# Optimization experiments

Measured on AMD Instinct MI355X. Metric: run time of the kernel, lower is better.

The kernel has to match this reference:

```python
import jax, jax.numpy as jnp
import numpy as np


def setup_inputs() -> dict:
    key = jax.random.key(0)
    k1, k2 = jax.random.split(key)
    B, D = 8192, 256
    pred = jax.random.normal(k1, (B, D), dtype=jnp.float32)
    gt = jax.random.normal(k2, (B, D), dtype=jnp.float32)
    sigma = jnp.ones((), dtype=jnp.float32)  # learned scalar param (dim=1, mode='auto')
    return {"pred": pred, "gt": gt, "sigma": sigma}


def reference(pred, gt, sigma):
    # p, g: [B, D] (flatten from start_dim=1 is identity for 2D inputs)
    p = pred.reshape(pred.shape[0], -1)
    g = gt.reshape(gt.shape[0], -1)
    B, D = p.shape
    noise_var = sigma ** 2
    # MVN(mean=p_i, cov=noise_var*I).log_prob(g_j) in closed form:
    # -0.5 * ||g_j - p_i||^2 / noise_var - 0.5 * D * log(2*pi*noise_var)
    sq_dist = (
        jnp.sum(p * p, axis=-1)[:, None]
        + jnp.sum(g * g, axis=-1)[None, :]
        - 2.0 * (p @ g.T)
    )  # [B, B]
    log_norm = 0.5 * D * jnp.log(2.0 * jnp.pi * noise_var)
    logits = -0.5 * sq_dist / noise_var - log_norm  # [B, B], class dim = 1
    # cross_entropy(logits, arange(B)) = mean_i(-log_softmax(logits)[i, i])
    logp = jax.nn.log_softmax(logits, axis=1)
    loss = -jnp.mean(jnp.diagonal(logp))
    loss = loss * jax.lax.stop_gradient(2.0 * noise_var)
    return loss
```

## Files before the change

### kernel.cpp

```cpp
#include <hip/hip_runtime.h>
#include <hip/hip_fp8.h>


typedef float f32x4 __attribute__((ext_vector_type(4)));
typedef long llong2 __attribute__((ext_vector_type(2)));

#define LN2F 0.6931471805599453f
#define LOG2EF 1.4426950408889634f
#define NB 8192
#define ND 256
#define NCHUNK 32

#define AS1 __attribute__((address_space(1)))
#define AS3 __attribute__((address_space(3)))

__device__ __forceinline__ float fexp2(float x) {
#if __has_builtin(__builtin_amdgcn_exp2f)
  return __builtin_amdgcn_exp2f(x);
#else
  float r;
  asm("v_exp_f32 %0, %1\n\ts_nop 1" : "=v"(r) : "v"(x));
  return r;
#endif
}

__device__ __forceinline__ int pack4_fp8(float a, float b, float c, float d) {
#if __has_builtin(__builtin_amdgcn_cvt_pk_fp8_f32)
  int w = __builtin_amdgcn_cvt_pk_fp8_f32(a, b, 0, false);
  w = __builtin_amdgcn_cvt_pk_fp8_f32(c, d, w, true);
  return w;
#else
  unsigned b0 = __hip_fp8_e4m3(a).__x, b1 = __hip_fp8_e4m3(b).__x;
  unsigned b2 = __hip_fp8_e4m3(c).__x, b3 = __hip_fp8_e4m3(d).__x;
  return (int)(b0 | (b1 << 8) | (b2 << 16) | (b3 << 24));
#endif
}

__global__ __launch_bounds__(256) void vmse_prep(
    const float* __restrict__ pred, const float* __restrict__ gt,
    const float* __restrict__ sigma,
    unsigned char* __restrict__ Ah, unsigned char* __restrict__ Bh,
    float* __restrict__ diag, float* __restrict__ gnorm,
    float* __restrict__ ghs)
{
  const float nv = sigma[0] * sigma[0];
  const float s = LOG2EF / nv;
  const int row = blockIdx.x * 4 + (threadIdx.x >> 6);
  const int l = threadIdx.x & 63;
  const float4 p = *(const float4*)(pred + row * ND + l * 4);
  const float4 g = *(const float4*)(gt   + row * ND + l * 4);
  const int pw = pack4_fp8(p.x * s, p.y * s, p.z * s, p.w * s);
  const int gw = pack4_fp8(g.x, g.y, g.z, g.w);
  const int pos = (l >> 4) * 64 + ((l & 7) >> 1) * 16 + ((l >> 3) & 1) * 8 + (l & 1) * 4;
  *(int*)(Ah + row * ND + pos) = pw;
  *(int*)(Bh + row * ND + pos) = gw;
  float dd = p.x * g.x + p.y * g.y + p.z * g.z + p.w * g.w;
  float gg = g.x * g.x + g.y * g.y + g.z * g.z + g.w * g.w;
  #pragma unroll
  for (int off = 1; off < 64; off <<= 1) {
    dd += __shfl_xor(dd, off);
    gg += __shfl_xor(gg, off);
  }
  if (l == 0) {
    diag[row] = dd;
    gnorm[row] = gg;
    ghs[row] = -0.5f * s * gg;
  }
}

__device__ __forceinline__ void epi(const f32x4 z, float& m, float& l) {
  const float tmax = fmaxf(fmaxf(z[0], z[1]), fmaxf(z[2], z[3]));
  if (__any(tmax > m + 8.0f)) {
    const float nm = fmaxf(m, tmax);
    l *= fexp2(m - nm);
    m = nm;
  }
  l += (fexp2(z[0] - m) + fexp2(z[1] - m)) + (fexp2(z[2] - m) + fexp2(z[3] - m));
}

__global__ __launch_bounds__(512, 4) void vmse_main(
    const unsigned char* __restrict__ Ah, const unsigned char* __restrict__ Bh,
    const float* __restrict__ ghs, float* __restrict__ partial)
{
  __shared__ unsigned char lds[8][32 * 256];
  __shared__ float lds_ghs[256];
  const int tid = threadIdx.x;
  const int lane = tid & 63;
  const int wid = tid >> 6;
  const int rb = blockIdx.x & 31;
  const int ch = blockIdx.x >> 5;
  const int r15 = lane & 15;
  const int hi = lane >> 4;
  const int j0 = ch * 256;

  {
    const int r = wid * 4 + (lane >> 4);
    const int cg = (lane & 15) ^ (r & 7);
    const unsigned char* src = Bh + (size_t)(j0 + r) * ND + cg * 16;
    #pragma unroll
    for (int t = 0; t < 8; ++t)
      __builtin_amdgcn_global_load_lds(
          (const AS1 unsigned int*)(src + t * 8192),
          (AS3 unsigned int*)&lds[t][wid * 1024], 16, 0, 0);
  }
  if (tid < 256) lds_ghs[tid] = ghs[j0 + tid];

  long pf[2][8];
  #pragma unroll
  for (int ns = 0; ns < 2; ++ns) {
    const unsigned char* prow =
        Ah + (size_t)((rb * 256) + (wid * 32) + (ns * 16) + r15) * ND;
    #pragma unroll
    for (int kk2 = 0; kk2 < 4; ++kk2) {
      const llong2 v = *(const llong2*)(prow + kk2 * 64 + hi * 16);
      pf[ns][2 * kk2] = v[0];
      pf[ns][2 * kk2 + 1] = v[1];
    }
  }

  const int r7 = r15 & 7;
  const int r7lo = r7 & 3, r7hi = r7 >> 2;
  const int h2 = hi ^ r7lo;
  const char* base = (const char*)&lds[0][0] + r15 * 256 + h2 * 16;
  const char* pE = base + r7hi * 64;
  const char* pO = base + 64 - r7hi * 64;

  float m2[2], l2[2];
  #pragma unroll
  for (int ns = 0; ns < 2; ++ns) { m2[ns] = -3.0e38f; l2[ns] = 0.0f; }

  #define COMPUTE(PE, PO, gp)                                                \
    {                                                                        \
      _Pragma("unroll")                                                      \
      for (int ms = 0; ms < 2; ++ms) {                                       \
        const f32x4 gv = *(const f32x4*)((gp) + ms * 64 + hi * 16);          \
        f32x4 a0 = gv;                                                       \
        f32x4 a1 = gv;                                                       \
        const llong2 gA = *(const llong2*)((PE) + ms * 4096);                \
        const llong2 gB = *(const llong2*)((PO) + ms * 4096);                \
        const llong2 gC = *(const llong2*)((PE) + ms * 4096 + 128);          \
        const llong2 gD = *(const llong2*)((PO) + ms * 4096 + 128);          \
        const long gf[8] = {gA[0], gA[1], gB[0], gB[1],                      \
                            gC[0], gC[1], gD[0], gD[1]};                     \
        __builtin_amdgcn_s_setprio(1);                                       \
        _Pragma("unroll")                                                    \
        for (int kk = 0; kk < 8; ++kk) {                                     \
          a0 = __builtin_amdgcn_mfma_f32_16x16x32_fp8_fp8(gf[kk], pf[0][kk], a0, 0, 0, 0); \
          a1 = __builtin_amdgcn_mfma_f32_16x16x32_fp8_fp8(gf[kk], pf[1][kk], a1, 0, 0, 0); \
        }                                                                    \
        __builtin_amdgcn_s_setprio(0);                                       \
        epi(a0, m2[0], l2[0]);                                               \
        epi(a1, m2[1], l2[1]);                                               \
      }                                                                      \
    }

  __syncthreads();

  const char* pEc = pE;
  const char* pOc = pO;
  const char* gp = (const char*)lds_ghs;
  for (int tt = 0; tt < 4; ++tt) {
    COMPUTE(pEc, pOc, gp);
    COMPUTE(pEc + 8192, pOc + 8192, gp + 128);
    pEc += 16384; pOc += 16384; gp += 256;
  }

  #pragma unroll
  for (int ns = 0; ns < 2; ++ns) {
    float m = m2[ns], l = l2[ns];
    #pragma unroll
    for (int off = 16; off <= 32; off <<= 1) {
      const float om = __shfl_xor(m, off);
      const float ol = __shfl_xor(l, off);
      const float nm = fmaxf(m, om);
      l = l * fexp2(m - nm) + ol * fexp2(om - nm);
      m = nm;
    }
    if (hi == 0) {
      const int row = rb * 256 + wid * 32 + ns * 16 + r15;
      partial[row * NCHUNK + ch] = m + log2f(l);
    }
  }
}

__global__ __launch_bounds__(256) void vmse_combine(
    const float* __restrict__ partial, const float* __restrict__ diag,
    const float* __restrict__ gnorm, const float* __restrict__ sigma,
    float* __restrict__ bsum)
{
  const int r = blockIdx.x * 256 + threadIdx.x;
  const float nv = sigma[0] * sigma[0];
  float p[NCHUNK];
  float M = -3.0e38f;
  #pragma unroll
  for (int c = 0; c < NCHUNK; ++c) { p[c] = partial[r * NCHUNK + c]; M = fmaxf(M, p[c]); }
  float ssum = 0.f;
  #pragma unroll
  for (int c = 0; c < NCHUNK; ++c) ssum += exp2f(p[c] - M);
  const float lse2 = M + log2f(ssum);
  const float zii = (diag[r] - 0.5f * gnorm[r]) / nv;
  float contrib = LN2F * lse2 - zii;
  #pragma unroll
  for (int off = 1; off < 64; off <<= 1) contrib += __shfl_xor(contrib, off);
  __shared__ float wsum[4];
  if ((threadIdx.x & 63) == 0) wsum[threadIdx.x >> 6] = contrib;
  __syncthreads();
  if (threadIdx.x == 0)
    bsum[blockIdx.x] = (wsum[0] + wsum[1]) + (wsum[2] + wsum[3]);
}

__global__ __launch_bounds__(64) void vmse_final(
    const float* __restrict__ bsum, const float* __restrict__ sigma,
    float* __restrict__ out)
{
  const int lane = threadIdx.x;
  float v = (lane < 32) ? bsum[lane] : 0.f;
  #pragma unroll
  for (int off = 1; off < 64; off <<= 1) v += __shfl_xor(v, off);
  if (lane == 0) {
    const float nv = sigma[0] * sigma[0];
    out[0] = v * (2.0f * nv / (float)NB);
  }
}

extern "C" void kernel_launch(void* const* d_in, const int* in_sizes, int n_in,
                              void* d_out, int out_size, void* d_ws, size_t ws_size,
                              hipStream_t stream)
{
  const float* pred  = (const float*)d_in[0];
  const float* gt    = (const float*)d_in[1];
  const float* sigma = (const float*)d_in[2];
  char* ws = (char*)d_ws;
  unsigned char* Ah = (unsigned char*)(ws);
  unsigned char* Bh = (unsigned char*)(ws + (2u << 20));
  float* gnorm   = (float*)(ws + (4u << 20));
  float* diag    = (float*)(ws + (4u << 20) + (32u << 10));
  float* ghs     = (float*)(ws + (4u << 20) + (64u << 10));
  float* partial = (float*)(ws + (4u << 20) + (96u << 10));
  float* bsum    = (float*)(ws + (4u << 20) + (96u << 10) + (1u << 20));

  vmse_prep<<<NB / 4, 256, 0, stream>>>(pred, gt, sigma, Ah, Bh, diag, gnorm, ghs);
  vmse_main<<<32 * NCHUNK, 512, 0, stream>>>(Ah, Bh, ghs, partial);
  vmse_combine<<<NB / 256, 256, 0, stream>>>(partial, diag, gnorm, sigma, bsum);
  vmse_final<<<1, 64, 0, stream>>>(bsum, sigma, (float*)d_out);
}
```

Before: 45.26 us.

## Switch main GEMM from 16x16x32 to 32x32x16 FP8 MFMA tiles

Replaces the pair of 16x16x32 FP8 MFMA accumulators per wave with a single 32x32x16 MFMA accumulator covering 32 rows by 32 columns. To match the new fragment shape it changes the FP8 packing layout in the prep kernel, the LDS swizzle, and the per-lane A-fragment loads. The online log-sum-exp epilogue now works on 16-element accumulators with one cross-half shuffle merge. This should cut LDS fragment loads per MFMA and give higher MFMA throughput per instruction, at the cost of a larger accumulator and more exp work per epilogue step.

```diff
diff --git a/kernel.cpp b/kernel.cpp
--- a/kernel.cpp
+++ b/kernel.cpp
@@ -3,6 +3,7 @@
 
 
 typedef float f32x4 __attribute__((ext_vector_type(4)));
+typedef float f32x16 __attribute__((ext_vector_type(16)));
 typedef long llong2 __attribute__((ext_vector_type(2)));
 
 #define LN2F 0.6931471805599453f
@@ -51,7 +52,7 @@
   const float4 g = *(const float4*)(gt   + row * ND + l * 4);
   const int pw = pack4_fp8(p.x * s, p.y * s, p.z * s, p.w * s);
   const int gw = pack4_fp8(g.x, g.y, g.z, g.w);
-  const int pos = (l >> 4) * 64 + ((l & 7) >> 1) * 16 + ((l >> 3) & 1) * 8 + (l & 1) * 4;
+  const int pos = (l >> 3) * 32 + ((l >> 1) & 1) * 16 + ((l >> 2) & 1) * 8 + (l & 1) * 4;
   *(int*)(Ah + row * ND + pos) = pw;
   *(int*)(Bh + row * ND + pos) = gw;
   float dd = p.x * g.x + p.y * g.y + p.z * g.z + p.w * g.w;
@@ -66,16 +67,6 @@
     gnorm[row] = gg;
     ghs[row] = -0.5f * s * gg;
   }
-}
-
-__device__ __forceinline__ void epi(const f32x4 z, float& m, float& l) {
-  const float tmax = fmaxf(fmaxf(z[0], z[1]), fmaxf(z[2], z[3]));
-  if (__any(tmax > m + 8.0f)) {
-    const float nm = fmaxf(m, tmax);
-    l *= fexp2(m - nm);
-    m = nm;
-  }
-  l += (fexp2(z[0] - m) + fexp2(z[1] - m)) + (fexp2(z[2] - m) + fexp2(z[3] - m));
 }
 
 __global__ __launch_bounds__(512, 4) void vmse_main(
@@ -89,8 +80,8 @@
   const int wid = tid >> 6;
   const int rb = blockIdx.x & 31;
   const int ch = blockIdx.x >> 5;
-  const int r15 = lane & 15;
-  const int hi = lane >> 4;
+  const int r31 = lane & 31;
+  const int hi = lane >> 5;
   const int j0 = ch * 256;
 
   {
@@ -105,80 +96,82 @@
   }
   if (tid < 256) lds_ghs[tid] = ghs[j0 + tid];
 
-  long pf[2][8];
-  #pragma unroll
-  for (int ns = 0; ns < 2; ++ns) {
-    const unsigned char* prow =
-        Ah + (size_t)((rb * 256) + (wid * 32) + (ns * 16) + r15) * ND;
-    #pragma unroll
-    for (int kk2 = 0; kk2 < 4; ++kk2) {
-      const llong2 v = *(const llong2*)(prow + kk2 * 64 + hi * 16);
-      pf[ns][2 * kk2] = v[0];
-      pf[ns][2 * kk2 + 1] = v[1];
-    }
-  }
-
-  const int r7 = r15 & 7;
-  const int r7lo = r7 & 3, r7hi = r7 >> 2;
-  const int h2 = hi ^ r7lo;
-  const char* base = (const char*)&lds[0][0] + r15 * 256 + h2 * 16;
-  const char* pE = base + r7hi * 64;
-  const char* pO = base + 64 - r7hi * 64;
-
-  float m2[2], l2[2];
-  #pragma unroll
-  for (int ns = 0; ns < 2; ++ns) { m2[ns] = -3.0e38f; l2[ns] = 0.0f; }
-
-  #define COMPUTE(PE, PO, gp)                                                \
-    {                                                                        \
-      _Pragma("unroll")                                                      \
-      for (int ms = 0; ms < 2; ++ms) {                                       \
-        const f32x4 gv = *(const f32x4*)((gp) + ms * 64 + hi * 16);          \
-        f32x4 a0 = gv;                                                       \
-        f32x4 a1 = gv;                                                       \
-        const llong2 gA = *(const llong2*)((PE) + ms * 4096);                \
-        const llong2 gB = *(const llong2*)((PO) + ms * 4096);                \
-        const llong2 gC = *(const llong2*)((PE) + ms * 4096 + 128);          \
-        const llong2 gD = *(const llong2*)((PO) + ms * 4096 + 128);          \
-        const long gf[8] = {gA[0], gA[1], gB[0], gB[1],                      \
-                            gC[0], gC[1], gD[0], gD[1]};                     \
-        __builtin_amdgcn_s_setprio(1);                                       \
-        _Pragma("unroll")                                                    \
-        for (int kk = 0; kk < 8; ++kk) {                                     \
-          a0 = __builtin_amdgcn_mfma_f32_16x16x32_fp8_fp8(gf[kk], pf[0][kk], a0, 0, 0, 0); \
-          a1 = __builtin_amdgcn_mfma_f32_16x16x32_fp8_fp8(gf[kk], pf[1][kk], a1, 0, 0, 0); \
-        }                                                                    \
-        __builtin_amdgcn_s_setprio(0);                                       \
-        epi(a0, m2[0], l2[0]);                                               \
-        epi(a1, m2[1], l2[1]);                                               \
-      }                                                                      \
-    }
+  long pf[16];
+  {
+    const unsigned char* prow = Ah + (size_t)((rb * 256) + (wid * 32) + r31) * ND;
+    #pragma unroll
+    for (int t2 = 0; t2 < 8; ++t2) {
+      const llong2 v = *(const llong2*)(prow + t2 * 32 + hi * 16);
+      pf[2 * t2] = v[0];
+      pf[2 * t2 + 1] = v[1];
+    }
+  }
+
+  const int r0b = r31 & 1;
+  const int q2 = (r31 >> 1) & 3;
+  const char* base = (const char*)&lds[0][0] + r31 * 256 + (hi ^ r0b) * 16;
+  const char* pq[4];
+  #pragma unroll
+  for (int b = 0; b < 4; ++b) pq[b] = base + ((b ^ q2) * 32);
+
+  float m2 = -3.0e38f, l2 = 0.0f;
 
   __syncthreads();
 
-  const char* pEc = pE;
-  const char* pOc = pO;
-  const char* gp = (const char*)lds_ghs;
-  for (int tt = 0; tt < 4; ++tt) {
-    COMPUTE(pEc, pOc, gp);
-    COMPUTE(pEc + 8192, pOc + 8192, gp + 128);
-    pEc += 16384; pOc += 16384; gp += 256;
-  }
-
-  #pragma unroll
-  for (int ns = 0; ns < 2; ++ns) {
-    float m = m2[ns], l = l2[ns];
-    #pragma unroll
-    for (int off = 16; off <= 32; off <<= 1) {
-      const float om = __shfl_xor(m, off);
-      const float ol = __shfl_xor(l, off);
-      const float nm = fmaxf(m, om);
-      l = l * fexp2(m - nm) + ol * fexp2(om - nm);
-      m = nm;
-    }
+  const char* gbase = (const char*)lds_ghs + hi * 16;
+  #pragma unroll
+  for (int tile = 0; tile < 8; ++tile) {
+    f32x16 acc;
+    #pragma unroll
+    for (int q = 0; q < 4; ++q) {
+      const f32x4 gv = *(const f32x4*)(gbase + tile * 128 + q * 32);
+      acc[4 * q + 0] = gv[0];
+      acc[4 * q + 1] = gv[1];
+      acc[4 * q + 2] = gv[2];
+      acc[4 * q + 3] = gv[3];
+    }
+    __builtin_amdgcn_s_setprio(1);
+    #pragma unroll
+    for (int a = 0; a < 2; ++a) {
+      #pragma unroll
+      for (int b = 0; b < 4; ++b) {
+        const llong2 g = *(const llong2*)(pq[b] + a * 128 + tile * 8192);
+        const int t = 2 * (a * 4 + b);
+        acc = __builtin_amdgcn_mfma_f32_32x32x16_fp8_fp8(g[0], pf[t], acc, 0, 0, 0);
+        acc = __builtin_amdgcn_mfma_f32_32x32x16_fp8_fp8(g[1], pf[t + 1], acc, 0, 0, 0);
+      }
+    }
+    __builtin_amdgcn_s_setprio(0);
+    float mx0 = fmaxf(fmaxf(acc[0], acc[1]), fmaxf(acc[2], acc[3]));
+    float mx1 = fmaxf(fmaxf(acc[4], acc[5]), fmaxf(acc[6], acc[7]));
+    float mx2 = fmaxf(fmaxf(acc[8], acc[9]), fmaxf(acc[10], acc[11]));
+    float mx3 = fmaxf(fmaxf(acc[12], acc[13]), fmaxf(acc[14], acc[15]));
+    const float tmax = fmaxf(fmaxf(mx0, mx1), fmaxf(mx2, mx3));
+    if (__any(tmax > m2 + 8.0f)) {
+      const float nm = fmaxf(m2, tmax);
+      l2 *= fexp2(m2 - nm);
+      m2 = nm;
+    }
+    float e0 = (fexp2(acc[0] - m2) + fexp2(acc[1] - m2)) +
+               (fexp2(acc[2] - m2) + fexp2(acc[3] - m2));
+    float e1 = (fexp2(acc[4] - m2) + fexp2(acc[5] - m2)) +
+               (fexp2(acc[6] - m2) + fexp2(acc[7] - m2));
+    float e2 = (fexp2(acc[8] - m2) + fexp2(acc[9] - m2)) +
+               (fexp2(acc[10] - m2) + fexp2(acc[11] - m2));
+    float e3 = (fexp2(acc[12] - m2) + fexp2(acc[13] - m2)) +
+               (fexp2(acc[14] - m2) + fexp2(acc[15] - m2));
+    l2 += (e0 + e1) + (e2 + e3);
+  }
+
+  {
+    const float om = __shfl_xor(m2, 32);
+    const float ol = __shfl_xor(l2, 32);
+    const float nm = fmaxf(m2, om);
+    l2 = l2 * fexp2(m2 - nm) + ol * fexp2(om - nm);
+    m2 = nm;
     if (hi == 0) {
-      const int row = rb * 256 + wid * 32 + ns * 16 + r15;
-      partial[row * NCHUNK + ch] = m + log2f(l);
+      const int row = rb * 256 + wid * 32 + r31;
+      partial[row * NCHUNK + ch] = m2 + log2f(l2);
     }
   }
 }
```

Result: no change. 44.38 us (-1.9%).
